# Kernel optimization log

Measured on AMD Instinct MI355X. Metric: run time of the kernel, lower is better.

Reference implementation:

```python
import jax, jax.numpy as jnp
import numpy as np

NUM_STUFF = 53
NUM_THING = 80
NUM_CLASSES = NUM_STUFF + NUM_THING  # 133
OBJ_THR = 0.4
OVERLAP_THR = 0.8
B, Q, HM, WM = 2, 100, 160, 160  # mask res = image/4


def setup_inputs() -> dict:
    key = jax.random.key(0)
    k1, k2 = jax.random.split(key)
    # Scale logits so some queries exceed the 0.4 softmax-score threshold.
    logits = 5.0 * jax.random.normal(k1, (B, Q, NUM_CLASSES + 1), dtype=jnp.float32)
    # Give each query a dominant blob (10x10 tile grid) so the greedy
    # overlap-threshold fusion accepts a realistic set of segments.
    th, tw = HM // 10, WM // 10
    tile_id = (jnp.arange(HM) // th)[:, None] * 10 + (jnp.arange(WM) // tw)[None, :]  # [HM,WM]
    bias = jnp.where(tile_id[None, :, :] == jnp.arange(Q)[:, None, None], 8.0, -8.0)  # [Q,HM,WM]
    noise = jax.random.normal(k2, (B, Q, HM, WM), dtype=jnp.float32)
    masks = noise + bias[None]
    return {"logits": logits, "masks": masks, "H": 640, "W": 640}


def reference(logits, masks, H, W):
    """Vectorized, jit-compatible port of Mask2FormerPanoptic._panoptic_merge.

    logits: [B, Q, C+1], masks: [B, Q, h, w]. Returns (sem_seg [B,C,H,W] f32,
    panoptic_seg [B,H,W] int32). The sequential greedy loop is equivalent to a
    per-query acceptance test (areas are loop-invariant) + cumsum id assignment,
    because argmax assigns each pixel to exactly one query.
    """
    Qn = masks.shape[1]

    def merge(lg, mk):
        probs = jax.nn.softmax(lg, axis=-1)               # [Q, C+1]
        scores = jnp.max(probs, axis=-1)                  # [Q]
        labels = jnp.argmax(probs, axis=-1)               # [Q]
        keep = (labels < NUM_CLASSES) & (scores > OBJ_THR)
        # sigmoid then bilinear upsample (half-pixel centers == align_corners=False)
        up = jax.image.resize(jax.nn.sigmoid(mk), (Qn, H, W), method='bilinear')  # [Q,H,W]
        prob_masks = jnp.where(keep[:, None, None], scores[:, None, None] * up, -1.0)
        mask_ids = jnp.argmax(prob_masks, axis=0)         # [H,W]
        mask_area = jnp.zeros((Qn,), jnp.int32).at[mask_ids.ravel()].add(1)  # [Q]
        orig_area = jnp.sum(up >= 0.5, axis=(1, 2))       # [Q]
        accepted = keep & (mask_area > 0) & (orig_area > 0) & (
            mask_area.astype(jnp.float32) > OVERLAP_THR * orig_area.astype(jnp.float32))
        ids = jnp.cumsum(accepted.astype(jnp.int32))      # greedy 1-based segment ids
        panoptic = jnp.where(accepted[mask_ids], ids[mask_ids], 0).astype(jnp.int32)
        masked = jnp.where(accepted[:, None, None], up, 0.0)
        # sem_seg[cls] = max over accepted queries with that class (zeros init)
        sem = jnp.zeros((NUM_CLASSES, H, W), jnp.float32).at[labels].max(masked)
        return sem, panoptic

    return jax.vmap(merge)(logits, masks)
```

## Files before the change

kernel.cpp:

```cpp
#include <hip/hip_runtime.h>
#include <stdint.h>
#include <math.h>

#define NB   2
#define NQ   100
#define NCLS 133
#define NCL1 134
#define HM   160
#define WM   160
#define HO   640
#define WO   640
#define G    8
#define NCELL (HM*WM)

static __device__ __forceinline__ int clampi(int v, int lo, int hi){ return v<lo?lo:(v>hi?hi:v); }
static __device__ __forceinline__ double dsig(float x){ return 1.0/(1.0+exp(-(double)x)); }

__global__ void k_classify(const float* __restrict__ logits, double* __restrict__ scores,
                           int* __restrict__ labels, int* __restrict__ keepf,
                           int* __restrict__ kq, int* __restrict__ Kc,
                           int* __restrict__ marea, int* __restrict__ oarea)
{
  int t = threadIdx.x;
  for (int i=t;i<NB*NQ;i+=blockDim.x){ marea[i]=0; oarea[i]=0; }
  if (t < NB*NQ){
    const float* l = logits + (size_t)t*NCL1;
    float mx = l[0]; int am = 0;
    for (int c=1;c<NCL1;++c){ float v=l[c]; if (v>mx){ mx=v; am=c; } }
    double s = 0.0;
    for (int c=0;c<NCL1;++c) s += exp((double)l[c] - (double)mx);
    double sc = 1.0/s;
    scores[t] = sc; labels[t] = am;
    keepf[t] = (am < NCLS && sc > 0.4) ? 1 : 0;
  }
  __syncthreads();
  if (t < NB){
    int k = 0;
    for (int q=0;q<NQ;++q) if (keepf[t*NQ+q]) kq[t*NQ + (k++)] = q;
    Kc[t] = k;
  }
}

__global__ void k_sigmoid32(const float* __restrict__ masks, float* __restrict__ sig32,
                            const int* __restrict__ keepf)
{
  int gid = blockIdx.x*blockDim.x + threadIdx.x;
  int bq  = gid / (HM*WM/4);
  if (!keepf[bq]) return;
  float4 v = reinterpret_cast<const float4*>(masks)[gid];
  float4 o;
  o.x = (float)dsig(v.x);
  o.y = (float)dsig(v.y);
  o.z = (float)dsig(v.z);
  o.w = (float)dsig(v.w);
  reinterpret_cast<float4*>(sig32)[gid] = o;
}

__global__ __launch_bounds__(128) void k_argmax_part(const float* __restrict__ masks,
        const double* __restrict__ scores, const int* __restrict__ kq,
        const int* __restrict__ Kc, double* __restrict__ pbest, uint8_t* __restrict__ pq,
        int* __restrict__ oarea)
{
  __shared__ double patch[2][10][18];
  __shared__ int oacc[16];
  const int b   = blockIdx.z / G;
  const int g   = blockIdx.z % G;
  const int tid = threadIdx.x;
  const int tx  = tid & 15, ty = tid >> 4;
  const int cj  = blockIdx.x*16 + tx;
  const int ci  = blockIdx.y*8  + ty;
  const int gr0 = blockIdx.y*8 - 1;
  const int gc0 = blockIdx.x*16 - 1;
  const int K   = Kc[b];
  const int Kg  = (K + G - 1) / G;
  const int k0  = g*Kg;
  const int k1  = min(K, k0 + Kg);

  if (tid < 16) oacc[tid] = 0;

  double best[4][4];
  int    bq[4][4];
  #pragma unroll
  for (int r=0;r<4;++r)
    #pragma unroll
    for (int s=0;s<4;++s){ best[r][s] = -1.0; bq[r][s] = 0; }

  if (k0 < k1){
    const float* mp = masks + (size_t)(b*NQ + kq[b*NQ+k0])*HM*WM;
    for (int i=tid;i<180;i+=128){
      int pr=i/18, pc=i-18*pr;
      patch[0][pr][pc] = dsig(mp[clampi(gr0+pr,0,HM-1)*WM + clampi(gc0+pc,0,WM-1)]);
    }
  }
  __syncthreads();

  for (int k=k0;k<k1;++k){
    const int    q  = kq[b*NQ+k];
    const double sc = scores[b*NQ+q];

    double pf0=0.0, pf1=0.0; int q2=-1;
    if (k+1 < k1){
      q2 = kq[b*NQ+k+1];
      const float* mp = masks + (size_t)(b*NQ + q2)*HM*WM;
      { int i=tid;      int pr=i/18, pc=i-18*pr;
        pf0 = dsig(mp[clampi(gr0+pr,0,HM-1)*WM + clampi(gc0+pc,0,WM-1)]); }
      if (tid+128 < 180){ int i=tid+128; int pr=i/18, pc=i-18*pr;
        pf1 = dsig(mp[clampi(gr0+pr,0,HM-1)*WM + clampi(gc0+pc,0,WM-1)]); }
    }

    const int cb = (k - k0) & 1;
    double v[3][3];
    #pragma unroll
    for (int rr=0;rr<3;++rr)
      #pragma unroll
      for (int cc=0;cc<3;++cc)
        v[rr][cc] = patch[cb][ty+rr][tx+cc];

    int cnt = 0;
    #pragma unroll
    for (int r=0;r<4;++r){
      const double wa = (r==0)?0.375:(r==1)?0.125:(r==2)?0.875:0.625;
      const double wb = (r==0)?0.625:(r==1)?0.875:(r==2)?0.125:0.375;
      const int ra = (r<2)?0:1, rb = ra+1;
      const bool vedge = (r<2) ? (ci==0) : (ci==HM-1);
      const int  vsel  = (r<2) ? rb : ra;
      double t0 = vedge ? v[vsel][0] : (wa*v[ra][0] + wb*v[rb][0]);
      double t1 = vedge ? v[vsel][1] : (wa*v[ra][1] + wb*v[rb][1]);
      double t2 = vedge ? v[vsel][2] : (wa*v[ra][2] + wb*v[rb][2]);
      double u[4];
      u[0] = (cj==0)    ? t1 : (0.375*t0 + 0.625*t1);
      u[1] = (cj==0)    ? t1 : (0.125*t0 + 0.875*t1);
      u[2] = (cj==WM-1) ? t1 : (0.875*t1 + 0.125*t2);
      u[3] = (cj==WM-1) ? t1 : (0.625*t1 + 0.375*t2);
      #pragma unroll
      for (int s=0;s<4;++s){
        cnt += (u[s] >= 0.5) ? 1 : 0;
        double val = sc*u[s];
        if (val > best[r][s]){ best[r][s] = val; bq[r][s] = q; }
      }
    }
    #pragma unroll
    for (int o2=32;o2>0;o2>>=1) cnt += __shfl_down(cnt, o2);
    if ((tid & 63) == 0) atomicAdd(&oacc[k-k0], cnt);

    if (q2 >= 0){
      { int i=tid;        patch[cb^1][i/18][i%18] = pf0; }
      if (tid+128 < 180){ int i=tid+128; patch[cb^1][i/18][i%18] = pf1; }
    }
    __syncthreads();
  }

  if (tid < k1-k0){
    int cv = oacc[tid];
    if (cv) atomicAdd(&oarea[b*NQ + kq[b*NQ+k0+tid]], cv);
  }

  const int cell = ci*WM + cj;
  #pragma unroll
  for (int r=0;r<4;++r)
    #pragma unroll
    for (int s=0;s<4;++s){
      size_t idx = ((size_t)((b*G + g)*16 + r*4 + s))*NCELL + cell;
      pbest[idx] = best[r][s];
      pq[idx]    = (uint8_t)bq[r][s];
    }
}

__global__ __launch_bounds__(128) void k_argmax_comb(const double* __restrict__ pbest,
        const uint8_t* __restrict__ pq, uint32_t* __restrict__ mids, int* __restrict__ marea)
{
  __shared__ int hist[NQ];
  const int b   = blockIdx.z;
  const int tid = threadIdx.x;
  const int tx  = tid & 15, ty = tid >> 4;
  const int cj  = blockIdx.x*16 + tx;
  const int ci  = blockIdx.y*8  + ty;
  const int cell= ci*WM + cj;

  for (int i=tid;i<NQ;i+=128) hist[i]=0;
  __syncthreads();

  int bqa[16];
  #pragma unroll
  for (int rs=0;rs<16;++rs){
    double cur = -1.0; int q = 0;
    #pragma unroll
    for (int g2=0;g2<G;++g2){
      size_t idx = ((size_t)((b*G + g2)*16 + rs))*NCELL + cell;
      double v = pbest[idx];
      if (v > cur){ cur = v; q = (int)pq[idx]; }
    }
    bqa[rs] = q;
  }

  #pragma unroll
  for (int r=0;r<4;++r){
    uint32_t w = (uint32_t)bqa[r*4+0] | ((uint32_t)bqa[r*4+1]<<8)
               | ((uint32_t)bqa[r*4+2]<<16) | ((uint32_t)bqa[r*4+3]<<24);
    int y = 4*ci + r;
    mids[(b*HO + y)*(WO/4) + cj] = w;
  }
  #pragma unroll
  for (int rs=0;rs<16;++rs)
    atomicAdd(&hist[bqa[rs]], 1);
  __syncthreads();
  for (int i=tid;i<NQ;i+=128)
    if (hist[i]) atomicAdd(&marea[b*NQ+i], hist[i]);
}

__global__ void k_finalize(const int* __restrict__ keepf, const int* __restrict__ labels,
                           const int* __restrict__ marea, const int* __restrict__ oarea,
                           float* __restrict__ fid, int* __restrict__ chanoff,
                           int* __restrict__ sortedq)
{
  const int b = blockIdx.x;
  const int tid = threadIdx.x;
  __shared__ int acc[NQ], lab[NQ], cntS[NCLS], start[NCLS];
  if (tid < NQ){
    int i = b*NQ + tid;
    int ma = marea[i], oa = oarea[i];
    acc[tid] = (keepf[i] && ma>0 && oa>0 && ((double)ma > 0.8*(double)oa)) ? 1 : 0;
    lab[tid] = labels[i];
  }
  if (tid < NCLS) cntS[tid]=0;
  __syncthreads();
  if (tid == 0){
    int A = 0;
    for (int q=0;q<NQ;++q){
      if (acc[q]){ A++; fid[b*NQ+q] = (float)A; cntS[lab[q]]++; }
      else fid[b*NQ+q] = 0.0f;
    }
    int off = 0;
    for (int c=0;c<NCLS;++c){ start[c]=off; chanoff[b*NCL1+c]=off; off += cntS[c]; }
    chanoff[b*NCL1+NCLS] = off;
    for (int q=0;q<NQ;++q)
      if (acc[q]){ int c=lab[q]; sortedq[b*NQ + start[c]] = q; start[c]++; }
  }
}

__global__ void k_pan(const uint32_t* __restrict__ mids, const float* __restrict__ fid,
                      float* __restrict__ out)
{
  int t = blockIdx.x*blockDim.x + threadIdx.x;
  int b = t / (HO*WO/4);
  uint32_t w = mids[t];
  float4 o;
  o.x = fid[b*NQ + (w & 255u)];
  o.y = fid[b*NQ + ((w>>8) & 255u)];
  o.z = fid[b*NQ + ((w>>16) & 255u)];
  o.w = fid[b*NQ + (w>>24)];
  reinterpret_cast<float4*>(out)[(size_t)NB*NCLS*(HO*(size_t)WO/4) + t] = o;
}

__global__ __launch_bounds__(256) void k_sem(const float* __restrict__ sig32,
        const int* __restrict__ chanoff, const int* __restrict__ sortedq,
        float* __restrict__ out)
{
  const int bc = blockIdx.z;
  const int b  = bc / NCLS, c = bc - b*NCLS;
  const int tid = threadIdx.x;
  const int tx  = tid & 15, ty = tid >> 4;
  const int cj  = blockIdx.x*16 + tx;
  const int ci  = blockIdx.y*16 + ty;
  const int s0 = chanoff[b*NCL1+c], s1 = chanoff[b*NCL1+c+1];

  float acc[4][4];
  #pragma unroll
  for (int r=0;r<4;++r)
    #pragma unroll
    for (int s=0;s<4;++s) acc[r][s]=0.f;

  if (s1 > s0){
    const int rm = max(ci-1,0), rp = min(ci+1,HM-1);
    const int cm = max(cj-1,0), cp = min(cj+1,WM-1);
    for (int i=s0;i<s1;++i){
      const int q = sortedq[b*NQ+i];
      const float* sp = sig32 + (size_t)(b*NQ+q)*HM*WM;
      float v[3][3];
      v[0][0]=sp[rm*WM+cm]; v[0][1]=sp[rm*WM+cj]; v[0][2]=sp[rm*WM+cp];
      v[1][0]=sp[ci*WM+cm]; v[1][1]=sp[ci*WM+cj]; v[1][2]=sp[ci*WM+cp];
      v[2][0]=sp[rp*WM+cm]; v[2][1]=sp[rp*WM+cj]; v[2][2]=sp[rp*WM+cp];
      #pragma unroll
      for (int r=0;r<4;++r){
        const float wa = (r==0)?0.375f:(r==1)?0.125f:(r==2)?0.875f:0.625f;
        const float wb = (r==0)?0.625f:(r==1)?0.875f:(r==2)?0.125f:0.375f;
        const int ra = (r<2)?0:1, rb = ra+1;
        const bool vedge = (r<2) ? (ci==0) : (ci==HM-1);
        const int  vsel  = (r<2) ? rb : ra;
        float t0 = vedge ? v[vsel][0] : (wa*v[ra][0] + wb*v[rb][0]);
        float t1 = vedge ? v[vsel][1] : (wa*v[ra][1] + wb*v[rb][1]);
        float t2 = vedge ? v[vsel][2] : (wa*v[ra][2] + wb*v[rb][2]);
        float u0 = (cj==0)    ? t1 : (0.375f*t0 + 0.625f*t1);
        float u1 = (cj==0)    ? t1 : (0.125f*t0 + 0.875f*t1);
        float u2 = (cj==WM-1) ? t1 : (0.875f*t1 + 0.125f*t2);
        float u3 = (cj==WM-1) ? t1 : (0.625f*t1 + 0.375f*t2);
        acc[r][0] = fmaxf(acc[r][0], u0);
        acc[r][1] = fmaxf(acc[r][1], u1);
        acc[r][2] = fmaxf(acc[r][2], u2);
        acc[r][3] = fmaxf(acc[r][3], u3);
      }
    }
  }
  #pragma unroll
  for (int r=0;r<4;++r){
    float4 o; o.x=acc[r][0]; o.y=acc[r][1]; o.z=acc[r][2]; o.w=acc[r][3];
    reinterpret_cast<float4*>(out)[((size_t)bc*HO + (4*ci+r))*(WO/4) + cj] = o;
  }
}

extern "C" void kernel_launch(void* const* d_in, const int* in_sizes, int n_in,
                              void* d_out, int out_size, void* d_ws, size_t ws_size,
                              hipStream_t stream)
{
  const float* logits = (const float*)d_in[0];
  const float* masks  = (const float*)d_in[1];
  float* out = (float*)d_out;

  char* ws = (char*)d_ws;
  size_t off = 0;
  auto alloc = [&](size_t bytes)->void*{
    void* p = ws + off; off = (off + bytes + 255) & ~(size_t)255; return p;
  };
  float*    sig32   = (float*)   alloc((size_t)NB*NQ*HM*WM*sizeof(float));
  double*   pbest   = (double*)  alloc((size_t)NB*G*16*NCELL*sizeof(double));
  uint8_t*  pq      = (uint8_t*) alloc((size_t)NB*G*16*NCELL*sizeof(uint8_t));
  uint32_t* mids    = (uint32_t*)alloc((size_t)NB*HO*(WO/4)*sizeof(uint32_t));
  double*   scores  = (double*)  alloc(NB*NQ*sizeof(double));
  int*      labels  = (int*)     alloc(NB*NQ*sizeof(int));
  int*      keepf   = (int*)     alloc(NB*NQ*sizeof(int));
  int*      kq      = (int*)     alloc(NB*NQ*sizeof(int));
  int*      Kc      = (int*)     alloc(NB*sizeof(int));
  int*      marea   = (int*)     alloc(NB*NQ*sizeof(int));
  int*      oarea   = (int*)     alloc(NB*NQ*sizeof(int));
  float*    fid     = (float*)   alloc(NB*NQ*sizeof(float));
  int*      chanoff = (int*)     alloc(NB*NCL1*sizeof(int));
  int*      sortedq = (int*)     alloc(NB*NQ*sizeof(int));

  hipLaunchKernelGGL(k_classify, dim3(1), dim3(256), 0, stream,
                     logits, scores, labels, keepf, kq, Kc, marea, oarea);
  hipLaunchKernelGGL(k_sigmoid32, dim3((NB*NQ*HM*WM/4)/256), dim3(256), 0, stream,
                     masks, sig32, keepf);
  hipLaunchKernelGGL(k_argmax_part, dim3(WM/16, HM/8, NB*G), dim3(128), 0, stream,
                     masks, scores, kq, Kc, pbest, pq, oarea);
  hipLaunchKernelGGL(k_argmax_comb, dim3(WM/16, HM/8, NB), dim3(128), 0, stream,
                     pbest, pq, mids, marea);
  hipLaunchKernelGGL(k_finalize, dim3(NB), dim3(192), 0, stream,
                     keepf, labels, marea, oarea, fid, chanoff, sortedq);
  hipLaunchKernelGGL(k_pan, dim3((NB*HO*WO/4)/256), dim3(256), 0, stream,
                     mids, fid, out);
  hipLaunchKernelGGL(k_sem, dim3(WM/16, HM/16, NB*NCLS), dim3(256), 0, stream,
                     sig32, chanoff, sortedq, out);
}
```

Measured before the change: 259.2 us.

## Give each wavefront a private halo patch and drop block-wide barriers in argmax loop

The argmax partial kernel moves from 128-thread blocks covering 16x8 cells to 256-thread blocks covering 16x16 cells. Each 64-lane wavefront now loads its own 6x18 halo patch of sigmoid values into a private LDS slot and uses it directly, with no cross-wave double buffering and no __syncthreads per query. This removes per-iteration block barriers and the software prefetch. In exchange the halo rows overlap more between waves, and the load latency of each query is no longer hidden by the prefetch. Correctness depends on intra-wavefront lockstep, since only compiler memory fences order the LDS writes and reads.

```diff
diff --git a/kernel.cpp b/kernel.cpp
--- a/kernel.cpp
+++ b/kernel.cpp
@@ -56,27 +56,31 @@
   reinterpret_cast<float4*>(sig32)[gid] = o;
 }
 
-__global__ __launch_bounds__(128) void k_argmax_part(const float* __restrict__ masks,
+__global__ __launch_bounds__(256) void k_argmax_part(const float* __restrict__ masks,
         const double* __restrict__ scores, const int* __restrict__ kq,
         const int* __restrict__ Kc, double* __restrict__ pbest, uint8_t* __restrict__ pq,
         int* __restrict__ oarea)
 {
-  __shared__ double patch[2][10][18];
+  __shared__ double patch[4][6][18];
   __shared__ int oacc[16];
-  const int b   = blockIdx.z / G;
-  const int g   = blockIdx.z % G;
-  const int tid = threadIdx.x;
-  const int tx  = tid & 15, ty = tid >> 4;
-  const int cj  = blockIdx.x*16 + tx;
-  const int ci  = blockIdx.y*8  + ty;
-  const int gr0 = blockIdx.y*8 - 1;
-  const int gc0 = blockIdx.x*16 - 1;
+  const int b    = blockIdx.z / G;
+  const int g    = blockIdx.z % G;
+  const int tid  = threadIdx.x;
+  const int lane = tid & 63;
+  const int w    = tid >> 6;
+  const int tx   = tid & 15, ty = tid >> 4;
+  const int wr   = ty & 3;
+  const int cj   = blockIdx.x*16 + tx;
+  const int ci   = blockIdx.y*16 + ty;
+  const int gr0  = blockIdx.y*16 + 4*w - 1;
+  const int gc0  = blockIdx.x*16 - 1;
   const int K   = Kc[b];
   const int Kg  = (K + G - 1) / G;
   const int k0  = g*Kg;
   const int k1  = min(K, k0 + Kg);
 
   if (tid < 16) oacc[tid] = 0;
+  __syncthreads();
 
   double best[4][4];
   int    bq[4][4];
@@ -85,36 +89,26 @@
     #pragma unroll
     for (int s=0;s<4;++s){ best[r][s] = -1.0; bq[r][s] = 0; }
 
-  if (k0 < k1){
-    const float* mp = masks + (size_t)(b*NQ + kq[b*NQ+k0])*HM*WM;
-    for (int i=tid;i<180;i+=128){
-      int pr=i/18, pc=i-18*pr;
-      patch[0][pr][pc] = dsig(mp[clampi(gr0+pr,0,HM-1)*WM + clampi(gc0+pc,0,WM-1)]);
-    }
-  }
-  __syncthreads();
+  const int i0 = lane,  p0r = i0/18, p0c = i0-18*p0r;
+  const int i1 = lane+64; int p1r = i1/18, p1c = i1-18*p1r;
+  const int a0 = clampi(gr0+p0r,0,HM-1)*WM + clampi(gc0+p0c,0,WM-1);
+  const int a1 = clampi(gr0+p1r,0,HM-1)*WM + clampi(gc0+p1c,0,WM-1);
 
   for (int k=k0;k<k1;++k){
     const int    q  = kq[b*NQ+k];
     const double sc = scores[b*NQ+q];
-
-    double pf0=0.0, pf1=0.0; int q2=-1;
-    if (k+1 < k1){
-      q2 = kq[b*NQ+k+1];
-      const float* mp = masks + (size_t)(b*NQ + q2)*HM*WM;
-      { int i=tid;      int pr=i/18, pc=i-18*pr;
-        pf0 = dsig(mp[clampi(gr0+pr,0,HM-1)*WM + clampi(gc0+pc,0,WM-1)]); }
-      if (tid+128 < 180){ int i=tid+128; int pr=i/18, pc=i-18*pr;
-        pf1 = dsig(mp[clampi(gr0+pr,0,HM-1)*WM + clampi(gc0+pc,0,WM-1)]); }
-    }
-
-    const int cb = (k - k0) & 1;
+    const float* mp = masks + (size_t)(b*NQ + q)*HM*WM;
+
+    patch[w][p0r][p0c] = dsig(mp[a0]);
+    if (lane < 44) patch[w][p1r][p1c] = dsig(mp[a1]);
+    asm volatile("" ::: "memory");
+
     double v[3][3];
     #pragma unroll
     for (int rr=0;rr<3;++rr)
       #pragma unroll
       for (int cc=0;cc<3;++cc)
-        v[rr][cc] = patch[cb][ty+rr][tx+cc];
+        v[rr][cc] = patch[w][wr+rr][tx+cc];
 
     int cnt = 0;
     #pragma unroll
@@ -141,15 +135,12 @@
     }
     #pragma unroll
     for (int o2=32;o2>0;o2>>=1) cnt += __shfl_down(cnt, o2);
-    if ((tid & 63) == 0) atomicAdd(&oacc[k-k0], cnt);
-
-    if (q2 >= 0){
-      { int i=tid;        patch[cb^1][i/18][i%18] = pf0; }
-      if (tid+128 < 180){ int i=tid+128; patch[cb^1][i/18][i%18] = pf1; }
-    }
-    __syncthreads();
-  }
-
+    if (lane == 0) atomicAdd(&oacc[k-k0], cnt);
+
+    asm volatile("" ::: "memory");
+  }
+
+  __syncthreads();
   if (tid < k1-k0){
     int cv = oacc[tid];
     if (cv) atomicAdd(&oarea[b*NQ + kq[b*NQ+k0+tid]], cv);
@@ -340,7 +331,7 @@
                      logits, scores, labels, keepf, kq, Kc, marea, oarea);
   hipLaunchKernelGGL(k_sigmoid32, dim3((NB*NQ*HM*WM/4)/256), dim3(256), 0, stream,
                      masks, sig32, keepf);
-  hipLaunchKernelGGL(k_argmax_part, dim3(WM/16, HM/8, NB*G), dim3(128), 0, stream,
+  hipLaunchKernelGGL(k_argmax_part, dim3(WM/16, HM/16, NB*G), dim3(256), 0, stream,
                      masks, scores, kq, Kc, pbest, pq, oarea);
   hipLaunchKernelGGL(k_argmax_comb, dim3(WM/16, HM/8, NB), dim3(128), 0, stream,
                      pbest, pq, mids, marea);
```

Result: no change. 260.2 us (+0.4%).
